# Optimization experiments

Hardware: AMD Instinct MI355X
Metric: run time of the kernel (lower is better)

Reference implementation:

```python
import jax, jax.numpy as jnp
import numpy as np

D = 512        # d_model
H = 8          # num_heads
DH = D // H    # d_head
HID = 2048     # ffn hidden
L = 6          # num_layers
S = 512        # src len
T = 512        # tgt len
VS = 16000     # src vocab
VT = 16000     # tgt vocab
B = 4
PAD = 0
EPS = 1e-5
SCALE = 0.02


def setup_inputs() -> dict:
    key = jax.random.key(0)
    ks = jax.random.split(key, 24)
    # tokens in [1, V), then force trailing pads
    src = jax.random.randint(ks[0], (B, S), 1, VS, dtype=jnp.int32).at[:, -32:].set(PAD)
    tgt = jax.random.randint(ks[1], (B, T), 1, VT, dtype=jnp.int32).at[:, -32:].set(PAD)
    n = lambda k, shp: (jax.random.normal(k, shp, dtype=jnp.float32) * SCALE)
    return {
        "src": src, "tgt": tgt,
        "emb_src": n(ks[2], (VS, D)),
        "emb_tgt": n(ks[3], (VT, D)),
        "enc_attn_w": n(ks[4], (L, 4, D, D)),
        "enc_attn_b": n(ks[5], (L, 4, D)),
        "enc_ff_w1": n(ks[6], (L, D, HID)),
        "enc_ff_b1": n(ks[7], (L, HID)),
        "enc_ff_w2": n(ks[8], (L, HID, D)),
        "enc_ff_b2": n(ks[9], (L, D)),
        "enc_ln_g": jnp.ones((L, 2, D), jnp.float32),
        "enc_ln_b": jnp.zeros((L, 2, D), jnp.float32),
        "dec_attn_w": n(ks[10], (L, 2, 4, D, D)),  # [:,0]=self, [:,1]=cross
        "dec_attn_b": n(ks[11], (L, 2, 4, D)),
        "dec_ff_w1": n(ks[12], (L, D, HID)),
        "dec_ff_b1": n(ks[13], (L, HID)),
        "dec_ff_w2": n(ks[14], (L, HID, D)),
        "dec_ff_b2": n(ks[15], (L, D)),
        "dec_ln_g": jnp.ones((L, 3, D), jnp.float32),
        "dec_ln_b": jnp.zeros((L, 3, D), jnp.float32),
        "fc_w": n(ks[16], (D, VT)),
        "fc_b": jnp.zeros((VT,), jnp.float32),
    }


def _pos_encoding(seq_len, d):
    pos = jnp.arange(seq_len, dtype=jnp.float32)[:, None]
    div = jnp.exp(jnp.arange(0, d, 2, dtype=jnp.float32) * (-np.log(10000.0) / d))
    pe = jnp.zeros((seq_len, d), jnp.float32)
    pe = pe.at[:, 0::2].set(jnp.sin(pos * div))
    pe = pe.at[:, 1::2].set(jnp.cos(pos * div))
    return pe


def _layer_norm(x, g, b):
    m = jnp.mean(x, axis=-1, keepdims=True)
    v = jnp.mean((x - m) ** 2, axis=-1, keepdims=True)
    return (x - m) / jnp.sqrt(v + EPS) * g + b


def _mha(xq, xkv, w, b, mask):
    # w: [4, D, D] (q,k,v,o), b: [4, D]; mask True = masked
    def proj(x, wi, bi):
        y = x @ wi + bi
        return y.reshape(y.shape[0], y.shape[1], H, DH).transpose(0, 2, 1, 3)  # [B,H,S,dh]
    Q, K, V = proj(xq, w[0], b[0]), proj(xkv, w[1], b[1]), proj(xkv, w[2], b[2])
    scores = jnp.einsum('bhqd,bhkd->bhqk', Q, K) / jnp.sqrt(jnp.float32(DH))
    if mask is not None:
        scores = jnp.where(mask, -jnp.inf, scores)
    attn = jax.nn.softmax(scores, axis=-1)
    out = jnp.einsum('bhqk,bhkd->bhqd', attn, V).transpose(0, 2, 1, 3).reshape(xq.shape[0], xq.shape[1], D)
    return out @ w[3] + b[3]


def reference(src, tgt, emb_src, emb_tgt,
              enc_attn_w, enc_attn_b, enc_ff_w1, enc_ff_b1, enc_ff_w2, enc_ff_b2,
              enc_ln_g, enc_ln_b,
              dec_attn_w, dec_attn_b, dec_ff_w1, dec_ff_b1, dec_ff_w2, dec_ff_b2,
              dec_ln_g, dec_ln_b, fc_w, fc_b):
    pe = _pos_encoding(max(S, T), D)
    enc = emb_src[src] + pe[:S]
    dec = emb_tgt[tgt] + pe[:T]
    src_mask = (src == PAD)[:, None, None, :]                        # [B,1,1,S]
    causal = jnp.triu(jnp.ones((T, T), bool), k=1)                   # [T,T]
    tgt_mask = causal[None, None] | (tgt == PAD)[:, None, None, :]   # [B,1,T,T]
    for l in range(L):
        a = _mha(enc, enc, enc_attn_w[l], enc_attn_b[l], src_mask)
        enc = _layer_norm(enc + a, enc_ln_g[l, 0], enc_ln_b[l, 0])
        f = jax.nn.relu(enc @ enc_ff_w1[l] + enc_ff_b1[l]) @ enc_ff_w2[l] + enc_ff_b2[l]
        enc = _layer_norm(enc + f, enc_ln_g[l, 1], enc_ln_b[l, 1])
    for l in range(L):
        a = _mha(dec, dec, dec_attn_w[l, 0], dec_attn_b[l, 0], tgt_mask)
        dec = _layer_norm(dec + a, dec_ln_g[l, 0], dec_ln_b[l, 0])
        a = _mha(dec, enc, dec_attn_w[l, 1], dec_attn_b[l, 1], src_mask)
        dec = _layer_norm(dec + a, dec_ln_g[l, 1], dec_ln_b[l, 1])
        f = jax.nn.relu(dec @ dec_ff_w1[l] + dec_ff_b1[l]) @ dec_ff_w2[l] + dec_ff_b2[l]
        dec = _layer_norm(dec + f, dec_ln_g[l, 2], dec_ln_b[l, 2])
    return dec @ fc_w + fc_b  # [B,T,VT]
```

## Files before the change

### kernel.cpp

```cpp
#include <hip/hip_runtime.h>
#include <math.h>

#define D 512
#define NH 8
#define DH 64
#define HID 2048
#define NL 6
#define SEQ 512
#define BATCH 4
#define MROWS (BATCH * SEQ)
#define NVT 16000
#define LNEPS 1e-5f

typedef __attribute__((ext_vector_type(8))) short short8;
typedef __attribute__((ext_vector_type(4))) float f32x4;

__device__ __forceinline__ ushort bf16_rtne(float f) {
    uint u = __builtin_bit_cast(uint, f);
    return (ushort)((u + 0x7fffu + ((u >> 16) & 1u)) >> 16);
}
__device__ __forceinline__ uint rtne2(float a, float b) {
    return (uint)bf16_rtne(a) | ((uint)bf16_rtne(b) << 16);
}

__global__ __launch_bounds__(256) void wsplit_kernel(const float* __restrict__ src,
                                                     ushort* __restrict__ dst,
                                                     int K, int N, size_t zstride) {
    __shared__ float T[64][65];
    src += (size_t)blockIdx.z * zstride;
    dst += (size_t)blockIdx.z * zstride;
    const int t = threadIdx.x;
    const int n0 = blockIdx.x * 64;
    const int k0 = blockIdx.y * 64;
    {
        const int kr = t >> 4, nc = (t & 15) * 4;
#pragma unroll
        for (int i = 0; i < 4; ++i) {
            float4 v = *(const float4*)&src[(size_t)(k0 + kr + 16 * i) * N + n0 + nc];
            T[kr + 16 * i][nc + 0] = v.x;
            T[kr + 16 * i][nc + 1] = v.y;
            T[kr + 16 * i][nc + 2] = v.z;
            T[kr + 16 * i][nc + 3] = v.w;
        }
    }
    __syncthreads();
    const int n = t >> 2;
    const int kc = (t & 3) * 16;
    uint h[8];
#pragma unroll
    for (int i = 0; i < 8; ++i)
        h[i] = rtne2(T[kc + 2 * i][n], T[kc + 2 * i + 1][n]);
    ushort* dh = &dst[(size_t)(n0 + n) * K + k0 + kc];
    *(uint4*)(dh + 0) = uint4{h[0], h[1], h[2], h[3]};
    *(uint4*)(dh + 8) = uint4{h[4], h[5], h[6], h[7]};
}

template <int BM, int BN, bool RELU>
__global__ __launch_bounds__(256) void gemm_mfma(const float* __restrict__ A0,
                                                 const float* __restrict__ A1,
                                                 const ushort* __restrict__ WT,
                                                 const float* __restrict__ bias,
                                                 float* __restrict__ C,
                                                 int M, int N, int K,
                                                 size_t wz, size_t cz) {
    constexpr int FM = BM / 32;
    constexpr int FN = BN / 32;
    constexpr int EA = BM / 32;
    constexpr int EB = BN / 64;
    constexpr int AROW = 40;

    __shared__ ushort Ah[2][BM * AROW];
    __shared__ ushort Bh[2][BN * AROW];

    const float* A = (blockIdx.z == 0) ? A0 : A1;
    WT += (size_t)blockIdx.z * wz;
    bias += (size_t)blockIdx.z * (size_t)N;
    C += (size_t)blockIdx.z * cz;

    const int tid = threadIdx.x;
    const int lane = tid & 63;
    const int wv = tid >> 6;
    const int wm = wv >> 1, wn = wv & 1;
    const int bm = blockIdx.x * BM;
    const int bn = blockIdx.y * BN;

    const int a_m = tid >> 3;
    const int a_kk = (tid & 7) * 4;
    const int b_n = tid >> 2;
    const int b_kq = (tid & 3) * 8;

    const float* aP[EA];
#pragma unroll
    for (int i = 0; i < EA; ++i)
        aP[i] = A + (size_t)(bm + 32 * i + a_m) * K + a_kk;
    const ushort* bP[EB];
#pragma unroll
    for (int i = 0; i < EB; ++i)
        bP[i] = WT + (size_t)(bn + 64 * i + b_n) * K + b_kq;

    f32x4 apre[EA];
    uint4 bpre[EB];
#pragma unroll
    for (int i = 0; i < EA; ++i) apre[i] = *(const f32x4*)(aP[i]);
#pragma unroll
    for (int i = 0; i < EB; ++i) bpre[i] = *(const uint4*)(bP[i]);

    f32x4 acc[FM][FN] = {};
    const int NT = K >> 5;

#pragma unroll
    for (int i = 0; i < EA; ++i) {
        const int idx = (32 * i + a_m) * AROW + a_kk;
        *(uint2*)&Ah[0][idx] = uint2{rtne2(apre[i][0], apre[i][1]),
                                     rtne2(apre[i][2], apre[i][3])};
    }
#pragma unroll
    for (int i = 0; i < EB; ++i)
        *(uint4*)&Bh[0][(64 * i + b_n) * AROW + b_kq] = bpre[i];
    if (NT > 1) {
#pragma unroll
        for (int i = 0; i < EA; ++i) apre[i] = *(const f32x4*)(aP[i] + 32);
#pragma unroll
        for (int i = 0; i < EB; ++i) bpre[i] = *(const uint4*)(bP[i] + 32);
    }
    __syncthreads();

    const int g8 = (lane >> 4) * 8;
    for (int t = 0; t < NT; ++t) {
        const int cur = t & 1;
        short8 af[FM], bf[FN];
#pragma unroll
        for (int mi = 0; mi < FM; ++mi)
            af[mi] = *(const short8*)&Ah[cur][(wm * (BM / 2) + mi * 16 + (lane & 15)) * AROW + g8];
#pragma unroll
        for (int ni = 0; ni < FN; ++ni)
            bf[ni] = *(const short8*)&Bh[cur][(wn * (BN / 2) + ni * 16 + (lane & 15)) * AROW + g8];
#pragma unroll
        for (int ni = 0; ni < FN; ++ni)
#pragma unroll
            for (int mi = 0; mi < FM; ++mi)
                acc[mi][ni] = __builtin_amdgcn_mfma_f32_16x16x32_bf16(af[mi], bf[ni], acc[mi][ni], 0, 0, 0);

        if (t + 1 < NT) {
#pragma unroll
            for (int i = 0; i < EA; ++i) {
                const int idx = (32 * i + a_m) * AROW + a_kk;
                *(uint2*)&Ah[cur ^ 1][idx] = uint2{rtne2(apre[i][0], apre[i][1]),
                                                   rtne2(apre[i][2], apre[i][3])};
            }
#pragma unroll
            for (int i = 0; i < EB; ++i)
                *(uint4*)&Bh[cur ^ 1][(64 * i + b_n) * AROW + b_kq] = bpre[i];
            if (t + 2 < NT) {
                const int ko = (t + 2) * 32;
#pragma unroll
                for (int i = 0; i < EA; ++i) apre[i] = *(const f32x4*)(aP[i] + ko);
#pragma unroll
                for (int i = 0; i < EB; ++i) bpre[i] = *(const uint4*)(bP[i] + ko);
            }
        }
        __syncthreads();
    }

#pragma unroll
    for (int ni = 0; ni < FN; ++ni) {
        const int col = bn + wn * (BN / 2) + ni * 16 + (lane & 15);
        const float bv = bias[col];
#pragma unroll
        for (int mi = 0; mi < FM; ++mi) {
            const int r0 = bm + wm * (BM / 2) + mi * 16 + (lane >> 4) * 4;
#pragma unroll
            for (int r = 0; r < 4; ++r) {
                float v = acc[mi][ni][r] + bv;
                if (RELU) v = fmaxf(v, 0.0f);
                C[(size_t)(r0 + r) * N + col] = v;
            }
        }
    }
}

template <int MODE>
__global__ __launch_bounds__(256) void attn_mfma(const float* __restrict__ Qm,
                                                 const float* __restrict__ Km,
                                                 const float* __restrict__ Vm,
                                                 const int* __restrict__ toks,
                                                 float* __restrict__ Om) {
    constexpr int ROW = 72;
    __shared__ ushort Kl[64 * ROW];
    __shared__ ushort Vl[64 * ROW];
    __shared__ ushort Pl[4][16 * ROW];

    const int tid = threadIdx.x;
    const int lane = tid & 63;
    const int w = tid >> 6;
    const int g = lane >> 4, c = lane & 15;
    const int b = blockIdx.y >> 3, h = blockIdx.y & 7;
    const int q0 = blockIdx.x * 64;
    const size_t base = (size_t)b * SEQ * D + h * DH;
    const int* tokp = toks + b * SEQ;

    short8 qf[2];
    {
        const float* qp = Qm + base + (size_t)(q0 + w * 16 + c) * D + g * 8;
#pragma unroll
        for (int kc = 0; kc < 2; ++kc) {
            union { ushort us[8]; short8 s8; } u;
#pragma unroll
            for (int i = 0; i < 8; ++i) u.us[i] = bf16_rtne(qp[kc * 32 + i]);
            qf[kc] = u.s8;
        }
    }

    const int sk_key = tid >> 2, sk_dh = (tid & 3) * 16;
    const int sv_dh = tid >> 2, sv_key = (tid & 3) * 16;
    const float* kP = Km + base + (size_t)sk_key * D + sk_dh;
    const float* vP = Vm + base + (size_t)sv_key * D + sv_dh;

    f32x4 kreg[4];
    float vreg[16];
#pragma unroll
    for (int j = 0; j < 4; ++j) kreg[j] = *(const f32x4*)(kP + 4 * j);
#pragma unroll
    for (int i = 0; i < 16; ++i) vreg[i] = vP[(size_t)i * D];

    f32x4 Ov[4] = {};
    float m_r[4], l_r[4];
#pragma unroll
    for (int r = 0; r < 4; ++r) { m_r[r] = -1e30f; l_r[r] = 0.f; }

    for (int kt = 0; kt < SEQ / 64; ++kt) {
        {
            union { ushort us[16]; uint4 u4[2]; } uk, uv;
#pragma unroll
            for (int j = 0; j < 4; ++j)
#pragma unroll
                for (int i = 0; i < 4; ++i) uk.us[4 * j + i] = bf16_rtne(kreg[j][i]);
#pragma unroll
            for (int i = 0; i < 16; ++i) uv.us[i] = bf16_rtne(vreg[i]);
            *(uint4*)&Kl[sk_key * ROW + sk_dh + 0] = uk.u4[0];
            *(uint4*)&Kl[sk_key * ROW + sk_dh + 8] = uk.u4[1];
            *(uint4*)&Vl[sv_dh * ROW + sv_key + 0] = uv.u4[0];
            *(uint4*)&Vl[sv_dh * ROW + sv_key + 8] = uv.u4[1];
        }
        __syncthreads();

        if (kt + 1 < SEQ / 64) {
            const size_t adv = (size_t)(kt + 1) * 64 * D;
#pragma unroll
            for (int j = 0; j < 4; ++j) kreg[j] = *(const f32x4*)(kP + adv + 4 * j);
#pragma unroll
            for (int i = 0; i < 16; ++i) vreg[i] = vP[adv + (size_t)i * D];
        }

        f32x4 sc[4] = {};
#pragma unroll
        for (int ni = 0; ni < 4; ++ni)
#pragma unroll
            for (int kc = 0; kc < 2; ++kc) {
                short8 kf = *(const short8*)&Kl[(ni * 16 + c) * ROW + kc * 32 + g * 8];
                sc[ni] = __builtin_amdgcn_mfma_f32_16x16x32_bf16(qf[kc], kf, sc[ni], 0, 0, 0);
            }

        const int k0g = kt * 64;
        int tk[4];
#pragma unroll
        for (int ni = 0; ni < 4; ++ni) tk[ni] = tokp[k0g + ni * 16 + c];
        float p[4][4], tm[4];
#pragma unroll
        for (int r = 0; r < 4; ++r) tm[r] = -1e30f;
#pragma unroll
        for (int ni = 0; ni < 4; ++ni) {
            const int key = k0g + ni * 16 + c;
            const bool colmask = (tk[ni] == 0);
#pragma unroll
            for (int r = 0; r < 4; ++r) {
                bool msk = colmask;
                if (MODE == 1) msk = msk || (key > q0 + w * 16 + 4 * g + r);
                const float s = msk ? -1e30f : sc[ni][r] * 0.125f;
                p[ni][r] = s;
                tm[r] = fmaxf(tm[r], s);
            }
        }
#pragma unroll
        for (int off = 1; off < 16; off <<= 1)
#pragma unroll
            for (int r = 0; r < 4; ++r) tm[r] = fmaxf(tm[r], __shfl_xor(tm[r], off, 16));
        float f_r[4], ts[4];
#pragma unroll
        for (int r = 0; r < 4; ++r) {
            const float mn = fmaxf(m_r[r], tm[r]);
            f_r[r] = __expf(m_r[r] - mn);
            m_r[r] = mn;
            ts[r] = 0.f;
        }
#pragma unroll
        for (int ni = 0; ni < 4; ++ni)
#pragma unroll
            for (int r = 0; r < 4; ++r) {
                const float e = (p[ni][r] <= -1e29f) ? 0.f : __expf(p[ni][r] - m_r[r]);
                p[ni][r] = e;
                ts[r] += e;
            }
#pragma unroll
        for (int off = 1; off < 16; off <<= 1)
#pragma unroll
            for (int r = 0; r < 4; ++r) ts[r] += __shfl_xor(ts[r], off, 16);
#pragma unroll
        for (int r = 0; r < 4; ++r) l_r[r] = l_r[r] * f_r[r] + ts[r];
#pragma unroll
        for (int nd = 0; nd < 4; ++nd)
#pragma unroll
            for (int r = 0; r < 4; ++r) Ov[nd][r] *= f_r[r];

#pragma unroll
        for (int ni = 0; ni < 4; ++ni)
#pragma unroll
            for (int r = 0; r < 4; ++r)
                Pl[w][(4 * r + g) * ROW + ni * 16 + c] = bf16_rtne(p[ni][r]);
        asm volatile("s_waitcnt lgkmcnt(0)" ::: "memory");
        __builtin_amdgcn_sched_barrier(0);

        const int pr = ((c & 3) << 2) | (c >> 2);
#pragma unroll
        for (int kc = 0; kc < 2; ++kc) {
            short8 pf = *(const short8*)&Pl[w][pr * ROW + kc * 32 + g * 8];
#pragma unroll
            for (int nd = 0; nd < 4; ++nd) {
                short8 vf = *(const short8*)&Vl[(nd * 16 + c) * ROW + kc * 32 + g * 8];
                Ov[nd] = __builtin_amdgcn_mfma_f32_16x16x32_bf16(pf, vf, Ov[nd], 0, 0, 0);
            }
        }
        __syncthreads();
    }

    float inv[4];
#pragma unroll
    for (int r = 0; r < 4; ++r) inv[r] = 1.0f / l_r[r];
    float* op = Om + base;
#pragma unroll
    for (int nd = 0; nd < 4; ++nd)
#pragma unroll
        for (int r = 0; r < 4; ++r)
            op[(size_t)(q0 + w * 16 + 4 * g + r) * D + nd * 16 + c] = Ov[nd][r] * inv[r];
}

__global__ __launch_bounds__(128) void embed2_kernel(const int* __restrict__ src,
                                                     const int* __restrict__ tgt,
                                                     const float* __restrict__ es,
                                                     const float* __restrict__ et,
                                                     float* __restrict__ xe,
                                                     float* __restrict__ xd) {
    const int which = blockIdx.y;
    const int* toks = which ? tgt : src;
    const float* emb = which ? et : es;
    float* out = which ? xd : xe;
    const int row = blockIdx.x;
    const int s = row & (SEQ - 1);
    const int tok = toks[row];
    const int d = threadIdx.x * 4;
    float4 e = *(const float4*)&emb[tok * D + d];
    float r[4];
#pragma unroll
    for (int i = 0; i < 4; i += 2) {
        const int dd = d + i;
        const float dv = expf((float)dd * (-9.210340371976184f / (float)D));
        const float ang = (float)s * dv;
        r[i] = sinf(ang);
        r[i + 1] = cosf(ang);
    }
    float4 o;
    o.x = e.x + r[0]; o.y = e.y + r[1]; o.z = e.z + r[2]; o.w = e.w + r[3];
    *(float4*)&out[row * D + d] = o;
}

__global__ __launch_bounds__(128) void add_ln_kernel(float* __restrict__ x,
                                                     const float* __restrict__ r,
                                                     const float* __restrict__ g,
                                                     const float* __restrict__ b) {
    const int row = blockIdx.x;
    const int t = threadIdx.x;
    const int d = t * 4;
    float4 xv = *(const float4*)&x[row * D + d];
    float4 rv = *(const float4*)&r[row * D + d];
    float4 v;
    v.x = xv.x + rv.x; v.y = xv.y + rv.y; v.z = xv.z + rv.z; v.w = xv.w + rv.w;
    float s = v.x + v.y + v.z + v.w;
    float s2 = v.x * v.x + v.y * v.y + v.z * v.z + v.w * v.w;
#pragma unroll
    for (int off = 32; off > 0; off >>= 1) {
        s += __shfl_down(s, off);
        s2 += __shfl_down(s2, off);
    }
    __shared__ float sh[4];
    if ((t & 63) == 0) { sh[(t >> 6) * 2] = s; sh[(t >> 6) * 2 + 1] = s2; }
    __syncthreads();
    s = sh[0] + sh[2];
    s2 = sh[1] + sh[3];
    const float mean = s * (1.0f / D);
    const float var = s2 * (1.0f / D) - mean * mean;
    const float rstd = rsqrtf(var + LNEPS);
    float4 gv = *(const float4*)&g[d];
    float4 bv = *(const float4*)&b[d];
    float4 o;
    o.x = (v.x - mean) * rstd * gv.x + bv.x;
    o.y = (v.y - mean) * rstd * gv.y + bv.y;
    o.z = (v.z - mean) * rstd * gv.z + bv.z;
    o.w = (v.w - mean) * rstd * gv.w + bv.w;
    *(float4*)&x[row * D + d] = o;
}

extern "C" void kernel_launch(void* const* d_in, const int* in_sizes, int n_in,
                              void* d_out, int out_size, void* d_ws, size_t ws_size,
                              hipStream_t stream) {
    const int* src = (const int*)d_in[0];
    const int* tgt = (const int*)d_in[1];
    const float* emb_src = (const float*)d_in[2];
    const float* emb_tgt = (const float*)d_in[3];
    const float* enc_attn_w = (const float*)d_in[4];
    const float* enc_attn_b = (const float*)d_in[5];
    const float* enc_ff_w1 = (const float*)d_in[6];
    const float* enc_ff_b1 = (const float*)d_in[7];
    const float* enc_ff_w2 = (const float*)d_in[8];
    const float* enc_ff_b2 = (const float*)d_in[9];
    const float* enc_ln_g = (const float*)d_in[10];
    const float* enc_ln_b = (const float*)d_in[11];
    const float* dec_attn_w = (const float*)d_in[12];
    const float* dec_attn_b = (const float*)d_in[13];
    const float* dec_ff_w1 = (const float*)d_in[14];
    const float* dec_ff_b1 = (const float*)d_in[15];
    const float* dec_ff_w2 = (const float*)d_in[16];
    const float* dec_ff_b2 = (const float*)d_in[17];
    const float* dec_ln_g = (const float*)d_in[18];
    const float* dec_ln_b = (const float*)d_in[19];
    const float* fc_w = (const float*)d_in[20];
    const float* fc_b = (const float*)d_in[21];
    float* out = (float*)d_out;

    float* ws = (float*)d_ws;
    const size_t NTOK = (size_t)MROWS * D;
    float* xe = ws;
    float* xd = xe + NTOK;
    float* qb = xd + NTOK;
    float* kb = qb + NTOK;
    float* vb = kb + NTOK;
    float* ab = vb + NTOK;
    float* tb = ab + NTOK;
    float* hb = tb + NTOK;
    ushort* u0 = (ushort*)(hb + (size_t)MROWS * HID);
    const size_t DD = (size_t)D * D;
    const size_t FCE = (size_t)D * NVT;
    const size_t act_bytes = (size_t)(7 * NTOK + (size_t)MROWS * HID) * 4;
    const bool batched = ws_size >= act_bytes + (168 * DD + FCE) * 2 + 1024;

    ushort *bEncA, *bEncF1, *bEncF2, *bDecA, *bDecF1, *bDecF2, *bFC;
    ushort *wA = nullptr, *wF1 = nullptr, *wF2 = nullptr;
    if (batched) {
        bEncA = u0;
        bEncF1 = bEncA + 24 * DD;
        bEncF2 = bEncF1 + 24 * DD;
        bDecA = bEncF2 + 24 * DD;
        bDecF1 = bDecA + 48 * DD;
        bDecF2 = bDecF1 + 24 * DD;
        bFC = bDecF2 + 24 * DD;
    } else {
        wA = u0;
        wF1 = wA + 8 * DD;
        wF2 = wF1 + 4 * DD;
        bFC = wF2 + 4 * DD;
        bEncA = bEncF1 = bEncF2 = bDecA = bDecF1 = bDecF2 = nullptr;
    }

    auto tr = [&](const float* w, ushort* dh, int K, int N, int nz) {
        dim3 grid(N / 64, K / 64, nz);
        wsplit_kernel<<<grid, 256, 0, stream>>>(w, dh, K, N, (size_t)K * N);
    };
    auto gemm64 = [&](const float* A, const ushort* WT,
                      const float* bias, float* C, int M, int N, int K) {
        dim3 grid(M / 64, N / 64, 1);
        gemm_mfma<64, 64, false><<<grid, 256, 0, stream>>>(A, A, WT, bias, C, M, N, K, 0, 0);
    };
    auto gemm128 = [&](const float* A, const ushort* WT,
                       const float* bias, float* C, int M, int N, int K, bool relu) {
        dim3 grid(M / 128, N / 128, 1);
        if (relu)
            gemm_mfma<128, 128, true><<<grid, 256, 0, stream>>>(A, A, WT, bias, C, M, N, K, 0, 0);
        else
            gemm_mfma<128, 128, false><<<grid, 256, 0, stream>>>(A, A, WT, bias, C, M, N, K, 0, 0);
    };
    auto gemm_qkv = [&](const float* Aq, const float* Akv,
                        const ushort* WT, const float* bi) {
        dim3 grid(MROWS / 64, D / 64, 3);
        gemm_mfma<64, 64, false><<<grid, 256, 0, stream>>>(Aq, Akv, WT, bi, qb,
                                                           MROWS, D, D, DD, NTOK);
    };

    if (batched) {
        tr(enc_attn_w, bEncA, D, D, 4 * NL);
        tr(enc_ff_w1, bEncF1, D, HID, NL);
        tr(enc_ff_w2, bEncF2, HID, D, NL);
        tr(dec_attn_w, bDecA, D, D, 8 * NL);
        tr(dec_ff_w1, bDecF1, D, HID, NL);
        tr(dec_ff_w2, bDecF2, HID, D, NL);
        tr(fc_w, bFC, D, NVT, 1);
    }

    embed2_kernel<<<dim3(MROWS, 2), 128, 0, stream>>>(src, tgt, emb_src, emb_tgt, xe, xd);

    const dim3 attn_grid(SEQ / 64, BATCH * NH);

    for (int l = 0; l < NL; ++l) {
        const float* bi = enc_attn_b + (size_t)l * 4 * D;
        ushort* eA;
        ushort* eF1;
        ushort* eF2;
        if (batched) {
            eA = bEncA + (size_t)l * 4 * DD;
            eF1 = bEncF1 + (size_t)l * 4 * DD;
            eF2 = bEncF2 + (size_t)l * 4 * DD;
        } else {
            eA = wA; eF1 = wF1; eF2 = wF2;
            tr(enc_attn_w + (size_t)l * 4 * DD, wA, D, D, 4);
            tr(enc_ff_w1 + (size_t)l * D * HID, wF1, D, HID, 1);
            tr(enc_ff_w2 + (size_t)l * HID * D, wF2, HID, D, 1);
        }

        gemm_qkv(xe, xe, eA, bi);
        attn_mfma<0><<<attn_grid, 256, 0, stream>>>(qb, kb, vb, src, ab);
        gemm64(ab, eA + 3 * DD, bi + 3 * D, tb, MROWS, D, D);
        add_ln_kernel<<<MROWS, 128, 0, stream>>>(xe, tb,
            enc_ln_g + (size_t)(l * 2 + 0) * D, enc_ln_b + (size_t)(l * 2 + 0) * D);
        gemm128(xe, eF1, enc_ff_b1 + (size_t)l * HID, hb, MROWS, HID, D, true);
        gemm64(hb, eF2, enc_ff_b2 + (size_t)l * D, tb, MROWS, D, HID);
        add_ln_kernel<<<MROWS, 128, 0, stream>>>(xe, tb,
            enc_ln_g + (size_t)(l * 2 + 1) * D, enc_ln_b + (size_t)(l * 2 + 1) * D);
    }

    for (int l = 0; l < NL; ++l) {
        ushort* dA;
        ushort* dF1;
        ushort* dF2;
        if (batched) {
            dA = bDecA + (size_t)l * 8 * DD;
            dF1 = bDecF1 + (size_t)l * 4 * DD;
            dF2 = bDecF2 + (size_t)l * 4 * DD;
        } else {
            dA = wA; dF1 = wF1; dF2 = wF2;
            tr(dec_attn_w + (size_t)l * 8 * DD, wA, D, D, 8);
            tr(dec_ff_w1 + (size_t)l * D * HID, wF1, D, HID, 1);
            tr(dec_ff_w2 + (size_t)l * HID * D, wF2, HID, D, 1);
        }
        {
            const float* bi = dec_attn_b + (size_t)(l * 2 + 0) * 4 * D;
            gemm_qkv(xd, xd, dA, bi);
            attn_mfma<1><<<attn_grid, 256, 0, stream>>>(qb, kb, vb, tgt, ab);
            gemm64(ab, dA + 3 * DD, bi + 3 * D, tb, MROWS, D, D);
            add_ln_kernel<<<MROWS, 128, 0, stream>>>(xd, tb,
                dec_ln_g + (size_t)(l * 3 + 0) * D, dec_ln_b + (size_t)(l * 3 + 0) * D);
        }
        {
            const float* bi = dec_attn_b + (size_t)(l * 2 + 1) * 4 * D;
            gemm_qkv(xd, xe, dA + 4 * DD, bi);
            attn_mfma<0><<<attn_grid, 256, 0, stream>>>(qb, kb, vb, src, ab);
            gemm64(ab, dA + 7 * DD, bi + 3 * D, tb, MROWS, D, D);
            add_ln_kernel<<<MROWS, 128, 0, stream>>>(xd, tb,
                dec_ln_g + (size_t)(l * 3 + 1) * D, dec_ln_b + (size_t)(l * 3 + 1) * D);
        }
        gemm128(xd, dF1, dec_ff_b1 + (size_t)l * HID, hb, MROWS, HID, D, true);
        gemm64(hb, dF2, dec_ff_b2 + (size_t)l * D, tb, MROWS, D, HID);
        add_ln_kernel<<<MROWS, 128, 0, stream>>>(xd, tb,
            dec_ln_g + (size_t)(l * 3 + 2) * D, dec_ln_b + (size_t)(l * 3 + 2) * D);
    }

    if (!batched) tr(fc_w, bFC, D, NVT, 1);
    {
        dim3 grid(MROWS / 128, NVT / 128, 1);
        gemm_mfma<128, 128, false><<<grid, 256, 0, stream>>>(xd, xd, bFC, fc_b, out,
                                                             MROWS, NVT, D, 0, 0);
    }
}
```

Measured before the change: 2.039 ms.

## Store intermediate activations in bf16 and single-buffer GEMM shared memory

Activations feeding GEMMs and attention (QKV, attention output, FFN hidden, and bf16 shadow copies of the residual stream written by embed and layernorm) are now stored as bf16 instead of fp32. This halves global memory traffic for those tensors and removes in-kernel fp32-to-bf16 conversion in the GEMM and attention loads. The GEMM kernel also drops its double-buffered LDS in favour of a single buffer with register prefetch, which adds a second barrier per K step and may reduce overlap. Layernorm and embed now write both fp32 and bf16 outputs, which adds some extra writes.

```diff
diff --git a/kernel.cpp b/kernel.cpp
--- a/kernel.cpp
+++ b/kernel.cpp
@@ -55,27 +55,26 @@
     *(uint4*)(dh + 8) = uint4{h[4], h[5], h[6], h[7]};
 }
 
-template <int BM, int BN, bool RELU>
-__global__ __launch_bounds__(256) void gemm_mfma(const float* __restrict__ A0,
-                                                 const float* __restrict__ A1,
+template <int BM, int BN, bool RELU, bool OBF16>
+__global__ __launch_bounds__(256) void gemm_mfma(const ushort* __restrict__ A0,
+                                                 const ushort* __restrict__ A1,
                                                  const ushort* __restrict__ WT,
                                                  const float* __restrict__ bias,
-                                                 float* __restrict__ C,
+                                                 void* __restrict__ Cv,
                                                  int M, int N, int K,
                                                  size_t wz, size_t cz) {
     constexpr int FM = BM / 32;
     constexpr int FN = BN / 32;
-    constexpr int EA = BM / 32;
+    constexpr int EA = BM / 64;
     constexpr int EB = BN / 64;
     constexpr int AROW = 40;
 
-    __shared__ ushort Ah[2][BM * AROW];
-    __shared__ ushort Bh[2][BN * AROW];
-
-    const float* A = (blockIdx.z == 0) ? A0 : A1;
+    __shared__ ushort Ah[BM * AROW];
+    __shared__ ushort Bh[BN * AROW];
+
+    const ushort* A = (blockIdx.z == 0) ? A0 : A1;
     WT += (size_t)blockIdx.z * wz;
     bias += (size_t)blockIdx.z * (size_t)N;
-    C += (size_t)blockIdx.z * cz;
 
     const int tid = threadIdx.x;
     const int lane = tid & 63;
@@ -84,81 +83,58 @@
     const int bm = blockIdx.x * BM;
     const int bn = blockIdx.y * BN;
 
-    const int a_m = tid >> 3;
-    const int a_kk = (tid & 7) * 4;
-    const int b_n = tid >> 2;
-    const int b_kq = (tid & 3) * 8;
-
-    const float* aP[EA];
+    const int s_r = tid >> 2;
+    const int s_k8 = (tid & 3) * 8;
+
+    const ushort* aP[EA];
 #pragma unroll
     for (int i = 0; i < EA; ++i)
-        aP[i] = A + (size_t)(bm + 32 * i + a_m) * K + a_kk;
+        aP[i] = A + (size_t)(bm + 64 * i + s_r) * K + s_k8;
     const ushort* bP[EB];
 #pragma unroll
     for (int i = 0; i < EB; ++i)
-        bP[i] = WT + (size_t)(bn + 64 * i + b_n) * K + b_kq;
-
-    f32x4 apre[EA];
-    uint4 bpre[EB];
-#pragma unroll
-    for (int i = 0; i < EA; ++i) apre[i] = *(const f32x4*)(aP[i]);
+        bP[i] = WT + (size_t)(bn + 64 * i + s_r) * K + s_k8;
+
+    uint4 apre[EA], bpre[EB];
+#pragma unroll
+    for (int i = 0; i < EA; ++i) apre[i] = *(const uint4*)(aP[i]);
 #pragma unroll
     for (int i = 0; i < EB; ++i) bpre[i] = *(const uint4*)(bP[i]);
 
     f32x4 acc[FM][FN] = {};
     const int NT = K >> 5;
-
-#pragma unroll
-    for (int i = 0; i < EA; ++i) {
-        const int idx = (32 * i + a_m) * AROW + a_kk;
-        *(uint2*)&Ah[0][idx] = uint2{rtne2(apre[i][0], apre[i][1]),
-                                     rtne2(apre[i][2], apre[i][3])};
-    }
-#pragma unroll
-    for (int i = 0; i < EB; ++i)
-        *(uint4*)&Bh[0][(64 * i + b_n) * AROW + b_kq] = bpre[i];
-    if (NT > 1) {
-#pragma unroll
-        for (int i = 0; i < EA; ++i) apre[i] = *(const f32x4*)(aP[i] + 32);
-#pragma unroll
-        for (int i = 0; i < EB; ++i) bpre[i] = *(const uint4*)(bP[i] + 32);
-    }
-    __syncthreads();
-
     const int g8 = (lane >> 4) * 8;
-    for (int t = 0; t < NT; ++t) {
-        const int cur = t & 1;
+
+    for (int kt = 0; kt < NT; ++kt) {
+#pragma unroll
+        for (int i = 0; i < EA; ++i)
+            *(uint4*)&Ah[(64 * i + s_r) * AROW + s_k8] = apre[i];
+#pragma unroll
+        for (int i = 0; i < EB; ++i)
+            *(uint4*)&Bh[(64 * i + s_r) * AROW + s_k8] = bpre[i];
+        __syncthreads();
+
+        if (kt + 1 < NT) {
+            const int ko = (kt + 1) * 32;
+#pragma unroll
+            for (int i = 0; i < EA; ++i) apre[i] = *(const uint4*)(aP[i] + ko);
+#pragma unroll
+            for (int i = 0; i < EB; ++i) bpre[i] = *(const uint4*)(bP[i] + ko);
+        }
+
         short8 af[FM], bf[FN];
 #pragma unroll
         for (int mi = 0; mi < FM; ++mi)
-            af[mi] = *(const short8*)&Ah[cur][(wm * (BM / 2) + mi * 16 + (lane & 15)) * AROW + g8];
+            af[mi] = *(const short8*)&Ah[(wm * (BM / 2) + mi * 16 + (lane & 15)) * AROW + g8];
 #pragma unroll
         for (int ni = 0; ni < FN; ++ni)
-            bf[ni] = *(const short8*)&Bh[cur][(wn * (BN / 2) + ni * 16 + (lane & 15)) * AROW + g8];
+            bf[ni] = *(const short8*)&Bh[(wn * (BN / 2) + ni * 16 + (lane & 15)) * AROW + g8];
+
 #pragma unroll
         for (int ni = 0; ni < FN; ++ni)
 #pragma unroll
             for (int mi = 0; mi < FM; ++mi)
                 acc[mi][ni] = __builtin_amdgcn_mfma_f32_16x16x32_bf16(af[mi], bf[ni], acc[mi][ni], 0, 0, 0);
-
-        if (t + 1 < NT) {
-#pragma unroll
-            for (int i = 0; i < EA; ++i) {
-                const int idx = (32 * i + a_m) * AROW + a_kk;
-                *(uint2*)&Ah[cur ^ 1][idx] = uint2{rtne2(apre[i][0], apre[i][1]),
-                                                   rtne2(apre[i][2], apre[i][3])};
-            }
-#pragma unroll
-            for (int i = 0; i < EB; ++i)
-                *(uint4*)&Bh[cur ^ 1][(64 * i + b_n) * AROW + b_kq] = bpre[i];
-            if (t + 2 < NT) {
-                const int ko = (t + 2) * 32;
-#pragma unroll
-                for (int i = 0; i < EA; ++i) apre[i] = *(const f32x4*)(aP[i] + ko);
-#pragma unroll
-                for (int i = 0; i < EB; ++i) bpre[i] = *(const uint4*)(bP[i] + ko);
-            }
-        }
         __syncthreads();
     }
 
@@ -173,18 +149,24 @@
             for (int r = 0; r < 4; ++r) {
                 float v = acc[mi][ni][r] + bv;
                 if (RELU) v = fmaxf(v, 0.0f);
-                C[(size_t)(r0 + r) * N + col] = v;
+                if (OBF16) {
+                    ushort* C = (ushort*)Cv + (size_t)blockIdx.z * cz;
+                    C[(size_t)(r0 + r) * N + col] = bf16_rtne(v);
+                } else {
+                    float* C = (float*)Cv + (size_t)blockIdx.z * cz;
+                    C[(size_t)(r0 + r) * N + col] = v;
+                }
             }
         }
     }
 }
 
 template <int MODE>
-__global__ __launch_bounds__(256) void attn_mfma(const float* __restrict__ Qm,
-                                                 const float* __restrict__ Km,
-                                                 const float* __restrict__ Vm,
+__global__ __launch_bounds__(256) void attn_mfma(const ushort* __restrict__ Qm,
+                                                 const ushort* __restrict__ Km,
+                                                 const ushort* __restrict__ Vm,
                                                  const int* __restrict__ toks,
-                                                 float* __restrict__ Om) {
+                                                 ushort* __restrict__ Om) {
     constexpr int ROW = 72;
     __shared__ ushort Kl[64 * ROW];
     __shared__ ushort Vl[64 * ROW];
@@ -201,25 +183,20 @@
 
     short8 qf[2];
     {
-        const float* qp = Qm + base + (size_t)(q0 + w * 16 + c) * D + g * 8;
-#pragma unroll
-        for (int kc = 0; kc < 2; ++kc) {
-            union { ushort us[8]; short8 s8; } u;
-#pragma unroll
-            for (int i = 0; i < 8; ++i) u.us[i] = bf16_rtne(qp[kc * 32 + i]);
-            qf[kc] = u.s8;
-        }
+        const ushort* qp = Qm + base + (size_t)(q0 + w * 16 + c) * D + g * 8;
+        qf[0] = *(const short8*)(qp);
+        qf[1] = *(const short8*)(qp + 32);
     }
 
     const int sk_key = tid >> 2, sk_dh = (tid & 3) * 16;
     const int sv_dh = tid >> 2, sv_key = (tid & 3) * 16;
-    const float* kP = Km + base + (size_t)sk_key * D + sk_dh;
-    const float* vP = Vm + base + (size_t)sv_key * D + sv_dh;
-
-    f32x4 kreg[4];
-    float vreg[16];
-#pragma unroll
-    for (int j = 0; j < 4; ++j) kreg[j] = *(const f32x4*)(kP + 4 * j);
+    const ushort* kP = Km + base + (size_t)sk_key * D + sk_dh;
+    const ushort* vP = Vm + base + (size_t)sv_key * D + sv_dh;
+
+    uint4 kreg[2];
+    ushort vreg[16];
+    kreg[0] = *(const uint4*)(kP);
+    kreg[1] = *(const uint4*)(kP + 8);
 #pragma unroll
     for (int i = 0; i < 16; ++i) vreg[i] = vP[(size_t)i * D];
 
@@ -230,15 +207,11 @@
 
     for (int kt = 0; kt < SEQ / 64; ++kt) {
         {
-            union { ushort us[16]; uint4 u4[2]; } uk, uv;
-#pragma unroll
-            for (int j = 0; j < 4; ++j)
-#pragma unroll
-                for (int i = 0; i < 4; ++i) uk.us[4 * j + i] = bf16_rtne(kreg[j][i]);
-#pragma unroll
-            for (int i = 0; i < 16; ++i) uv.us[i] = bf16_rtne(vreg[i]);
-            *(uint4*)&Kl[sk_key * ROW + sk_dh + 0] = uk.u4[0];
-            *(uint4*)&Kl[sk_key * ROW + sk_dh + 8] = uk.u4[1];
+            union { ushort us[16]; uint4 u4[2]; } uv;
+#pragma unroll
+            for (int i = 0; i < 16; ++i) uv.us[i] = vreg[i];
+            *(uint4*)&Kl[sk_key * ROW + sk_dh + 0] = kreg[0];
+            *(uint4*)&Kl[sk_key * ROW + sk_dh + 8] = kreg[1];
             *(uint4*)&Vl[sv_dh * ROW + sv_key + 0] = uv.u4[0];
             *(uint4*)&Vl[sv_dh * ROW + sv_key + 8] = uv.u4[1];
         }
@@ -246,8 +219,8 @@
 
         if (kt + 1 < SEQ / 64) {
             const size_t adv = (size_t)(kt + 1) * 64 * D;
-#pragma unroll
-            for (int j = 0; j < 4; ++j) kreg[j] = *(const f32x4*)(kP + adv + 4 * j);
+            kreg[0] = *(const uint4*)(kP + adv);
+            kreg[1] = *(const uint4*)(kP + adv + 8);
 #pragma unroll
             for (int i = 0; i < 16; ++i) vreg[i] = vP[adv + (size_t)i * D];
         }
@@ -336,12 +309,13 @@
     float inv[4];
 #pragma unroll
     for (int r = 0; r < 4; ++r) inv[r] = 1.0f / l_r[r];
-    float* op = Om + base;
+    ushort* op = Om + base;
 #pragma unroll
     for (int nd = 0; nd < 4; ++nd)
 #pragma unroll
         for (int r = 0; r < 4; ++r)
-            op[(size_t)(q0 + w * 16 + 4 * g + r) * D + nd * 16 + c] = Ov[nd][r] * inv[r];
+            op[(size_t)(q0 + w * 16 + 4 * g + r) * D + nd * 16 + c] =
+                bf16_rtne(Ov[nd][r] * inv[r]);
 }
 
 __global__ __launch_bounds__(128) void embed2_kernel(const int* __restrict__ src,
@@ -349,11 +323,14 @@
                                                      const float* __restrict__ es,
                                                      const float* __restrict__ et,
                                                      float* __restrict__ xe,
-                                                     float* __restrict__ xd) {
+                                                     float* __restrict__ xd,
+                                                     ushort* __restrict__ xeb,
+                                                     ushort* __restrict__ xdb) {
     const int which = blockIdx.y;
     const int* toks = which ? tgt : src;
     const float* emb = which ? et : es;
     float* out = which ? xd : xe;
+    ushort* outb = which ? xdb : xeb;
     const int row = blockIdx.x;
     const int s = row & (SEQ - 1);
     const int tok = toks[row];
@@ -371,9 +348,11 @@
     float4 o;
     o.x = e.x + r[0]; o.y = e.y + r[1]; o.z = e.z + r[2]; o.w = e.w + r[3];
     *(float4*)&out[row * D + d] = o;
+    *(uint2*)&outb[row * D + d] = uint2{rtne2(o.x, o.y), rtne2(o.z, o.w)};
 }
 
 __global__ __launch_bounds__(128) void add_ln_kernel(float* __restrict__ x,
+                                                     ushort* __restrict__ xb,
                                                      const float* __restrict__ r,
                                                      const float* __restrict__ g,
                                                      const float* __restrict__ b) {
@@ -407,6 +386,7 @@
     o.z = (v.z - mean) * rstd * gv.z + bv.z;
     o.w = (v.w - mean) * rstd * gv.w + bv.w;
     *(float4*)&x[row * D + d] = o;
+    *(uint2*)&xb[row * D + d] = uint2{rtne2(o.x, o.y), rtne2(o.z, o.w)};
 }
 
 extern "C" void kernel_launch(void* const* d_in, const int* in_sizes, int n_in,
@@ -440,16 +420,18 @@
     const size_t NTOK = (size_t)MROWS * D;
     float* xe = ws;
     float* xd = xe + NTOK;
-    float* qb = xd + NTOK;
-    float* kb = qb + NTOK;
-    float* vb = kb + NTOK;
-    float* ab = vb + NTOK;
-    float* tb = ab + NTOK;
-    float* hb = tb + NTOK;
-    ushort* u0 = (ushort*)(hb + (size_t)MROWS * HID);
+    float* tb = xd + NTOK;
+    ushort* xeb = (ushort*)(tb + NTOK);
+    ushort* xdb = xeb + NTOK;
+    ushort* qbb = xdb + NTOK;
+    ushort* kbb = qbb + NTOK;
+    ushort* vbb = kbb + NTOK;
+    ushort* abb = vbb + NTOK;
+    ushort* hbb = abb + NTOK;
+    ushort* u0 = hbb + 4 * NTOK;
     const size_t DD = (size_t)D * D;
     const size_t FCE = (size_t)D * NVT;
-    const size_t act_bytes = (size_t)(7 * NTOK + (size_t)MROWS * HID) * 4;
+    const size_t act_bytes = NTOK * (3 * 4 + 10 * 2);
     const bool batched = ws_size >= act_bytes + (168 * DD + FCE) * 2 + 1024;
 
     ushort *bEncA, *bEncF1, *bEncF2, *bDecA, *bDecF1, *bDecF2, *bFC;
@@ -474,24 +456,21 @@
         dim3 grid(N / 64, K / 64, nz);
         wsplit_kernel<<<grid, 256, 0, stream>>>(w, dh, K, N, (size_t)K * N);
     };
-    auto gemm64 = [&](const float* A, const ushort* WT,
-                      const float* bias, float* C, int M, int N, int K) {
+    auto gemm64f = [&](const ushort* A, const ushort* WT,
+                       const float* bias, float* C, int M, int N, int K) {
         dim3 grid(M / 64, N / 64, 1);
-        gemm_mfma<64, 64, false><<<grid, 256, 0, stream>>>(A, A, WT, bias, C, M, N, K, 0, 0);
+        gemm_mfma<64, 64, false, false><<<grid, 256, 0, stream>>>(A, A, WT, bias, C, M, N, K, 0, 0);
     };
-    auto gemm128 = [&](const float* A, const ushort* WT,
-                       const float* bias, float* C, int M, int N, int K, bool relu) {
+    auto gemm128_relu_b = [&](const ushort* A, const ushort* WT,
+                              const float* bias, ushort* C, int M, int N, int K) {
         dim3 grid(M / 128, N / 128, 1);
-        if (relu)
-            gemm_mfma<128, 128, true><<<grid, 256, 0, stream>>>(A, A, WT, bias, C, M, N, K, 0, 0);
-        else
-            gemm_mfma<128, 128, false><<<grid, 256, 0, stream>>>(A, A, WT, bias, C, M, N, K, 0, 0);
+        gemm_mfma<128, 128, true, true><<<grid, 256, 0, stream>>>(A, A, WT, bias, C, M, N, K, 0, 0);
     };
-    auto gemm_qkv = [&](const float* Aq, const float* Akv,
+    auto gemm_qkv = [&](const ushort* Aq, const ushort* Akv,
                         const ushort* WT, const float* bi) {
         dim3 grid(MROWS / 64, D / 64, 3);
-        gemm_mfma<64, 64, false><<<grid, 256, 0, stream>>>(Aq, Akv, WT, bi, qb,
-                                                           MROWS, D, D, DD, NTOK);
+        gemm_mfma<64, 64, false, true><<<grid, 256, 0, stream>>>(Aq, Akv, WT, bi, qbb,
+                                                                 MROWS, D, D, DD, NTOK);
     };
 
     if (batched) {
@@ -504,15 +483,14 @@
         tr(fc_w, bFC, D, NVT, 1);
     }
 
-    embed2_kernel<<<dim3(MROWS, 2), 128, 0, stream>>>(src, tgt, emb_src, emb_tgt, xe, xd);
+    embed2_kernel<<<dim3(MROWS, 2), 128, 0, stream>>>(src, tgt, emb_src, emb_tgt,
+                                                      xe, xd, xeb, xdb);
 
     const dim3 attn_grid(SEQ / 64, BATCH * NH);
 
     for (int l = 0; l < NL; ++l) {
         const float* bi = enc_attn_b + (size_t)l * 4 * D;
-        ushort* eA;
-        ushort* eF1;
-        ushort* eF2;
+        ushort *eA, *eF1, *eF2;
         if (batched) {
             eA = bEncA + (size_t)l * 4 * DD;
             eF1 = bEncF1 + (size_t)l * 4 * DD;
@@ -524,21 +502,19 @@
             tr(enc_ff_w2 + (size_t)l * HID * D, wF2, HID, D, 1);
         }
 
-        gemm_qkv(xe, xe, eA, bi);
-        attn_mfma<0><<<attn_grid, 256, 0, stream>>>(qb, kb, vb, src, ab);
-        gemm64(ab, eA + 3 * DD, bi + 3 * D, tb, MROWS, D, D);
-        add_ln_kernel<<<MROWS, 128, 0, stream>>>(xe, tb,
+        gemm_qkv(xeb, xeb, eA, bi);
+        attn_mfma<0><<<attn_grid, 256, 0, stream>>>(qbb, kbb, vbb, src, abb);
+        gemm64f(abb, eA + 3 * DD, bi + 3 * D, tb, MROWS, D, D);
+        add_ln_kernel<<<MROWS, 128, 0, stream>>>(xe, xeb, tb,
             enc_ln_g + (size_t)(l * 2 + 0) * D, enc_ln_b + (size_t)(l * 2 + 0) * D);
-        gemm128(xe, eF1, enc_ff_b1 + (size_t)l * HID, hb, MROWS, HID, D, true);
-        gemm64(hb, eF2, enc_ff_b2 + (size_t)l * D, tb, MROWS, D, HID);
-        add_ln_kernel<<<MROWS, 128, 0, stream>>>(xe, tb,
+        gemm128_relu_b(xeb, eF1, enc_ff_b1 + (size_t)l * HID, hbb, MROWS, HID, D);
+        gemm64f(hbb, eF2, enc_ff_b2 + (size_t)l * D, tb, MROWS, D, HID);
+        add_ln_kernel<<<MROWS, 128, 0, stream>>>(xe, xeb, tb,
             enc_ln_g + (size_t)(l * 2 + 1) * D, enc_ln_b + (size_t)(l * 2 + 1) * D);
     }
 
     for (int l = 0; l < NL; ++l) {
-        ushort* dA;
-        ushort* dF1;
-        ushort* dF2;
+        ushort *dA, *dF1, *dF2;
         if (batched) {
             dA = bDecA + (size_t)l * 8 * DD;
             dF1 = bDecF1 + (size_t)l * 4 * DD;
@@ -551,30 +527,30 @@
         }
         {
             const float* bi = dec_attn_b + (size_t)(l * 2 + 0) * 4 * D;
-            gemm_qkv(xd, xd, dA, bi);
-            attn_mfma<1><<<attn_grid, 256, 0, stream>>>(qb, kb, vb, tgt, ab);
-            gemm64(ab, dA + 3 * DD, bi + 3 * D, tb, MROWS, D, D);
-            add_ln_kernel<<<MROWS, 128, 0, stream>>>(xd, tb,
+            gemm_qkv(xdb, xdb, dA, bi);
+            attn_mfma<1><<<attn_grid, 256, 0, stream>>>(qbb, kbb, vbb, tgt, abb);
+            gemm64f(abb, dA + 3 * DD, bi + 3 * D, tb, MROWS, D, D);
+            add_ln_kernel<<<MROWS, 128, 0, stream>>>(xd, xdb, tb,
                 dec_ln_g + (size_t)(l * 3 + 0) * D, dec_ln_b + (size_t)(l * 3 + 0) * D);
         }
         {
             const float* bi = dec_attn_b + (size_t)(l * 2 + 1) * 4 * D;
-            gemm_qkv(xd, xe, dA + 4 * DD, bi);
-            attn_mfma<0><<<attn_grid, 256, 0, stream>>>(qb, kb, vb, src, ab);
-            gemm64(ab, dA + 7 * DD, bi + 3 * D, tb, MROWS, D, D);
-            add_ln_kernel<<<MROWS, 128, 0, stream>>>(xd, tb,
+            gemm_qkv(xdb, xeb, dA + 4 * DD, bi);
+            attn_mfma<0><<<attn_grid, 256, 0, stream>>>(qbb, kbb, vbb, src, abb);
+            gemm64f(abb, dA + 7 * DD, bi + 3 * D, tb, MROWS, D, D);
+            add_ln_kernel<<<MROWS, 128, 0, stream>>>(xd, xdb, tb,
                 dec_ln_g + (size_t)(l * 3 + 1) * D, dec_ln_b + (size_t)(l * 3 + 1) * D);
         }
-        gemm128(xd, dF1, dec_ff_b1 + (size_t)l * HID, hb, MROWS, HID, D, true);
-        gemm64(hb, dF2, dec_ff_b2 + (size_t)l * D, tb, MROWS, D, HID);
-        add_ln_kernel<<<MROWS, 128, 0, stream>>>(xd, tb,
+        gemm128_relu_b(xdb, dF1, dec_ff_b1 + (size_t)l * HID, hbb, MROWS, HID, D);
+        gemm64f(hbb, dF2, dec_ff_b2 + (size_t)l * D, tb, MROWS, D, HID);
+        add_ln_kernel<<<MROWS, 128, 0, stream>>>(xd, xdb, tb,
             dec_ln_g + (size_t)(l * 3 + 2) * D, dec_ln_b + (size_t)(l * 3 + 2) * D);
     }
 
     if (!batched) tr(fc_w, bFC, D, NVT, 1);
     {
         dim3 grid(MROWS / 128, NVT / 128, 1);
-        gemm_mfma<128, 128, false><<<grid, 256, 0, stream>>>(xd, xd, bFC, fc_b, out,
-                                                             MROWS, NVT, D, 0, 0);
-    }
-}
+        gemm_mfma<128, 128, false, false><<<grid, 256, 0, stream>>>(xdb, xdb, bFC, fc_b, out,
+                                                                    MROWS, NVT, D, 0, 0);
+    }
+}
```

New measurement: 2.116 ms. 3.8% more time.
